# Performance work log

Measured on AMD Instinct MI355X. Metric: run time of the kernel, lower is better.

The kernel has to match this reference:

```python
import jax, jax.numpy as jnp
import numpy as np

NUM_NODES = 500000
EMB = 200        # embedding_size
U = 32           # embedding_u_size
T = 4            # edge_type_count
DIM_A = 32
B = 16384        # batch of training pairs
NN = 10          # sampled neighbors per edge type


def setup_inputs() -> dict:
    key = jax.random.key(0)
    ks = jax.random.split(key, 8)
    inv_sqrt_e = 1.0 / np.sqrt(EMB).astype(np.float32)
    return {
        "train_inputs": jax.random.randint(ks[0], (B,), 0, NUM_NODES, dtype=jnp.int32),
        "train_types": jax.random.randint(ks[1], (B,), 0, T, dtype=jnp.int32),
        "node_neigh": jax.random.randint(ks[2], (B, T, NN), 0, NUM_NODES, dtype=jnp.int32),
        # learned parameters (init matches reset_parameters)
        "node_embeddings": jax.random.uniform(ks[3], (NUM_NODES, EMB), minval=-1.0, maxval=1.0, dtype=jnp.float32),
        "node_type_embeddings": jax.random.uniform(ks[4], (NUM_NODES, T, U), minval=-1.0, maxval=1.0, dtype=jnp.float32),
        "trans_weights": jax.random.normal(ks[5], (T, U, EMB), dtype=jnp.float32) * inv_sqrt_e,
        "trans_weights_s1": jax.random.normal(ks[6], (T, U, DIM_A), dtype=jnp.float32) * inv_sqrt_e,
        "trans_weights_s2": jax.random.normal(ks[7], (T, DIM_A, 1), dtype=jnp.float32) * inv_sqrt_e,
    }


def reference(train_inputs, train_types, node_neigh,
              node_embeddings, node_type_embeddings,
              trans_weights, trans_weights_s1, trans_weights_s2):
    # Per-edge-type neighbor aggregation (copy_src + sum in the DGL code):
    # for layer l: sum_n node_type_embeddings[node_neigh[b, l, n], l, :]
    layer_idx = jnp.arange(T, dtype=node_neigh.dtype)[None, :, None]      # [1,T,1]
    neigh = node_type_embeddings[node_neigh, layer_idx, :]                # [B,T,NN,U] gather
    node_type_embed = neigh.sum(axis=2)                                   # [B,T,U]

    tw  = trans_weights[train_types]                                      # [B,U,EMB]
    tw1 = trans_weights_s1[train_types]                                   # [B,U,A]
    tw2 = trans_weights_s2[train_types][..., 0]                           # [B,A]

    # attention over edge types
    h = jnp.tanh(jnp.einsum('btu,bua->bta', node_type_embed, tw1))        # [B,T,A]
    scores = jnp.einsum('bta,ba->bt', h, tw2)                             # [B,T]
    att = jax.nn.softmax(scores, axis=1)                                  # [B,T]
    comb = jnp.einsum('bt,btu->bu', att, node_type_embed)                 # [B,U]

    node_embed = node_embeddings[train_inputs] + jnp.einsum('bu,bue->be', comb, tw)  # [B,EMB]
    norm = jnp.maximum(jnp.linalg.norm(node_embed, axis=1, keepdims=True), 1e-12)
    return node_embed / norm
```

## Files before the change

### kernel.cpp

```cpp
#include <hip/hip_runtime.h>

#define EMB 200
#define U_DIM 32
#define T_DIM 4
#define DIM_A 32
#define NN 10
#define WAVES 4

__global__ __launch_bounds__(WAVES * 64) void gatne_kernel(
    const int* __restrict__ train_inputs,
    const int* __restrict__ train_types,
    const int* __restrict__ node_neigh,
    const float* __restrict__ node_emb,
    const float* __restrict__ node_type_emb,
    const float* __restrict__ tw,
    const float* __restrict__ tw1,
    const float* __restrict__ tw2,
    float* __restrict__ out)
{
    __shared__ float s_nte[WAVES][T_DIM][U_DIM];
    __shared__ float s_comb[WAVES][U_DIM];

    const int wid  = threadIdx.x >> 6;
    const int lane = threadIdx.x & 63;
    const int u    = lane & 31;
    const int th   = lane >> 5;
    const int b    = blockIdx.x * WAVES + wid;

    const int type = train_types[b];

    int my_neigh = 0;
    if (lane < T_DIM * NN) my_neigh = node_neigh[b * T_DIM * NN + lane];

    #pragma unroll
    for (int tt = 0; tt < 2; ++tt) {
        const int t = tt * 2 + th;
        float acc = 0.f;
        #pragma unroll
        for (int n = 0; n < NN; ++n) {
            const int idx = __shfl(my_neigh, t * NN + n, 64);
            acc += node_type_emb[((long)idx * T_DIM + t) * U_DIM + u];
        }
        s_nte[wid][t][u] = acc;
    }
    __syncthreads();

    const float* tw1p = tw1 + type * U_DIM * DIM_A;
    const float  w2   = tw2[type * DIM_A + u];
    float sc[2];
    #pragma unroll
    for (int tt = 0; tt < 2; ++tt) {
        const int t = tt * 2 + th;
        float acc = 0.f;
        #pragma unroll
        for (int uu = 0; uu < U_DIM; ++uu)
            acc += s_nte[wid][t][uu] * tw1p[uu * DIM_A + u];
        float s = tanhf(acc) * w2;
        #pragma unroll
        for (int m = 1; m < 32; m <<= 1) s += __shfl_xor(s, m, 64);
        sc[tt] = s;
    }
    const float o0 = __shfl_xor(sc[0], 32, 64);
    const float o1 = __shfl_xor(sc[1], 32, 64);
    const float s0 = th ? o0    : sc[0];
    const float s1 = th ? sc[0] : o0;
    const float s2 = th ? o1    : sc[1];
    const float s3 = th ? sc[1] : o1;

    const float mx = fmaxf(fmaxf(s0, s1), fmaxf(s2, s3));
    const float e0 = expf(s0 - mx), e1 = expf(s1 - mx);
    const float e2 = expf(s2 - mx), e3 = expf(s3 - mx);
    const float inv = 1.f / (e0 + e1 + e2 + e3);

    const float comb = (e0 * s_nte[wid][0][u] + e1 * s_nte[wid][1][u] +
                        e2 * s_nte[wid][2][u] + e3 * s_nte[wid][3][u]) * inv;
    s_comb[wid][u] = comb;
    __syncthreads();

    const int    node = train_inputs[b];
    const float* twp  = tw + type * U_DIM * EMB;

    float4 v = make_float4(0.f, 0.f, 0.f, 0.f);
    float sumsq = 0.f;
    if (lane < EMB / 4) {
        v = *(const float4*)(node_emb + (long)node * EMB + lane * 4);
        #pragma unroll
        for (int uu = 0; uu < U_DIM; ++uu) {
            const float  c = s_comb[wid][uu];
            const float4 w = *(const float4*)(twp + uu * EMB + lane * 4);
            v.x += c * w.x; v.y += c * w.y; v.z += c * w.z; v.w += c * w.w;
        }
        sumsq = v.x * v.x + v.y * v.y + v.z * v.z + v.w * v.w;
    }
    #pragma unroll
    for (int m = 1; m < 64; m <<= 1) sumsq += __shfl_xor(sumsq, m, 64);

    const float rinv = 1.f / fmaxf(sqrtf(sumsq), 1e-12f);
    if (lane < EMB / 4) {
        float4 o = make_float4(v.x * rinv, v.y * rinv, v.z * rinv, v.w * rinv);
        *(float4*)(out + (long)b * EMB + lane * 4) = o;
    }
}

extern "C" void kernel_launch(void* const* d_in, const int* in_sizes, int n_in,
                              void* d_out, int out_size, void* d_ws, size_t ws_size,
                              hipStream_t stream) {
    const int*   train_inputs = (const int*)d_in[0];
    const int*   train_types  = (const int*)d_in[1];
    const int*   node_neigh   = (const int*)d_in[2];
    const float* node_emb     = (const float*)d_in[3];
    const float* node_type_e  = (const float*)d_in[4];
    const float* tw           = (const float*)d_in[5];
    const float* tw1          = (const float*)d_in[6];
    const float* tw2          = (const float*)d_in[7];
    float*       out          = (float*)d_out;

    const int B = in_sizes[0];
    const int blocks = B / WAVES;

    gatne_kernel<<<blocks, WAVES * 64, 0, stream>>>(
        train_inputs, train_types, node_neigh,
        node_emb, node_type_e, tw, tw1, tw2, out);
}
```

Baseline: 40.17 us.

## Sort batch by edge type and tile trans_weights projection over 16 rows

Splits the fused kernel into a type bucketing pass (count, prefix, scatter into a padded permutation), an attention kernel that writes the combined U-vector to workspace, and an embed kernel where each wave handles 16 same-type rows. Grouping by type lets each trans_weights load be reused across 16 rows instead of reloaded once per row. The cost is six launches instead of one, an extra round trip of the comb vectors through global memory, and 16 float4 accumulators per lane, which raises register pressure.

```diff
diff --git a/kernel.cpp b/kernel.cpp
--- a/kernel.cpp
+++ b/kernel.cpp
@@ -7,19 +7,74 @@
 #define NN 10
 #define WAVES 4
 
-__global__ __launch_bounds__(WAVES * 64) void gatne_kernel(
-    const int* __restrict__ train_inputs,
+
+__global__ __launch_bounds__(256) void k_init(int* __restrict__ perm, int* __restrict__ cnt, int pb) {
+    int i = blockIdx.x * 256 + threadIdx.x;
+    if (i < pb) perm[i] = -1;
+    if (i < 4) cnt[i] = 0;
+}
+
+__global__ __launch_bounds__(1024) void k_count(const int* __restrict__ types, int* __restrict__ cnt) {
+    __shared__ int h[4];
+    const int tid = threadIdx.x;
+    if (tid < 4) h[tid] = 0;
+    __syncthreads();
+    const int b = blockIdx.x * 1024 + tid;
+    const int ty = types[b];
+    const int lane = tid & 63;
+    #pragma unroll
+    for (int tt = 0; tt < 4; ++tt) {
+        if (ty == tt) {
+            unsigned long long m = __ballot(1);
+            if (lane == __ffsll((long long)m) - 1) atomicAdd(&h[tt], __popcll(m));
+        }
+    }
+    __syncthreads();
+    if (tid < 4) atomicAdd(&cnt[tid], h[tid]);
+}
+
+__global__ void k_base(const int* __restrict__ cnt, int* __restrict__ fill) {
+    if (threadIdx.x == 0 && blockIdx.x == 0) {
+        int f = 0;
+        #pragma unroll
+        for (int t = 0; t < 4; ++t) { fill[t] = f; f += (cnt[t] + 15) & ~15; }
+    }
+}
+
+__global__ __launch_bounds__(1024) void k_scatter(const int* __restrict__ types,
+                                                  int* __restrict__ fill, int* __restrict__ perm) {
+    __shared__ int h[4], gb[4], woff[16][4];
+    const int tid = threadIdx.x;
+    const int wv = tid >> 6, lane = tid & 63;
+    if (tid < 4) h[tid] = 0;
+    __syncthreads();
+    const int b = blockIdx.x * 1024 + tid;
+    const int ty = types[b];
+    int rank = 0;
+    #pragma unroll
+    for (int tt = 0; tt < 4; ++tt) {
+        if (ty == tt) {
+            unsigned long long m = __ballot(1);
+            rank = __popcll(m & ((1ull << lane) - 1));
+            if (lane == __ffsll((long long)m) - 1) woff[wv][tt] = atomicAdd(&h[tt], __popcll(m));
+        }
+    }
+    __syncthreads();
+    if (tid < 4) gb[tid] = atomicAdd(&fill[tid], h[tid]);
+    __syncthreads();
+    perm[gb[ty] + woff[wv][ty] + rank] = b;
+}
+
+
+__global__ __launch_bounds__(WAVES * 64) void k_comb(
     const int* __restrict__ train_types,
     const int* __restrict__ node_neigh,
-    const float* __restrict__ node_emb,
     const float* __restrict__ node_type_emb,
-    const float* __restrict__ tw,
     const float* __restrict__ tw1,
     const float* __restrict__ tw2,
-    float* __restrict__ out)
+    float* __restrict__ combw)
 {
     __shared__ float s_nte[WAVES][T_DIM][U_DIM];
-    __shared__ float s_comb[WAVES][U_DIM];
 
     const int wid  = threadIdx.x >> 6;
     const int lane = threadIdx.x & 63;
@@ -74,33 +129,90 @@
 
     const float comb = (e0 * s_nte[wid][0][u] + e1 * s_nte[wid][1][u] +
                         e2 * s_nte[wid][2][u] + e3 * s_nte[wid][3][u]) * inv;
-    s_comb[wid][u] = comb;
-    __syncthreads();
-
-    const int    node = train_inputs[b];
-    const float* twp  = tw + type * U_DIM * EMB;
-
-    float4 v = make_float4(0.f, 0.f, 0.f, 0.f);
-    float sumsq = 0.f;
-    if (lane < EMB / 4) {
-        v = *(const float4*)(node_emb + (long)node * EMB + lane * 4);
-        #pragma unroll
-        for (int uu = 0; uu < U_DIM; ++uu) {
-            const float  c = s_comb[wid][uu];
-            const float4 w = *(const float4*)(twp + uu * EMB + lane * 4);
-            v.x += c * w.x; v.y += c * w.y; v.z += c * w.z; v.w += c * w.w;
-        }
-        sumsq = v.x * v.x + v.y * v.y + v.z * v.z + v.w * v.w;
-    }
-    #pragma unroll
-    for (int m = 1; m < 64; m <<= 1) sumsq += __shfl_xor(sumsq, m, 64);
-
-    const float rinv = 1.f / fmaxf(sqrtf(sumsq), 1e-12f);
-    if (lane < EMB / 4) {
-        float4 o = make_float4(v.x * rinv, v.y * rinv, v.z * rinv, v.w * rinv);
-        *(float4*)(out + (long)b * EMB + lane * 4) = o;
-    }
-}
+    if (lane < 32) combw[(size_t)b * 32 + lane] = comb;
+}
+
+
+__global__ __launch_bounds__(WAVES * 64) void k_embed(
+    const int* __restrict__ train_inputs,
+    const int* __restrict__ train_types,
+    const int* __restrict__ perm,
+    const float* __restrict__ combw,
+    const float* __restrict__ node_emb,
+    const float* __restrict__ tw,
+    float* __restrict__ out)
+{
+    __shared__ float4 s_comb4[WAVES][16][8];
+    __shared__ int s_bg[WAVES][16];
+    __shared__ int s_node[WAVES][16];
+
+    const int wid  = threadIdx.x >> 6;
+    const int lane = threadIdx.x & 63;
+    const int g = lane >> 2, q = lane & 3;
+    const long base16 = (long)(blockIdx.x * WAVES + wid) * 16;
+
+    const int bg = perm[base16 + g];
+    const bool valid = bg >= 0;
+    float4 c0 = make_float4(0.f, 0.f, 0.f, 0.f), c1 = c0;
+    if (valid) {
+        const float4* cp = (const float4*)(combw + (size_t)bg * 32 + q * 8);
+        c0 = cp[0]; c1 = cp[1];
+    }
+    s_comb4[wid][g][q * 2]     = c0;
+    s_comb4[wid][g][q * 2 + 1] = c1;
+    if (q == 0) { s_bg[wid][g] = bg; s_node[wid][g] = valid ? train_inputs[bg] : -1; }
+    const int tyv = valid ? train_types[bg] : 0;
+    const unsigned long long vm = __ballot(valid);
+    __syncthreads();
+    if (vm == 0ull) return;
+    const int t0 = __shfl(tyv, (int)(__ffsll((long long)vm) - 1), 64);
+
+    const int  c   = lane;
+    const bool act = c < EMB / 4;
+
+    float4 nv[16];
+    #pragma unroll
+    for (int gg = 0; gg < 16; ++gg) {
+        const int nd = s_node[wid][gg];
+        float4 t = make_float4(0.f, 0.f, 0.f, 0.f);
+        if (act && nd >= 0) t = *(const float4*)(node_emb + (size_t)nd * EMB + c * 4);
+        nv[gg] = t;
+    }
+
+    const float* twp = tw + (size_t)t0 * U_DIM * EMB + c * 4;
+    const float* scp = (const float*)&s_comb4[wid][0][0];
+    float4 acc[16];
+    #pragma unroll
+    for (int gg = 0; gg < 16; ++gg) acc[gg] = make_float4(0.f, 0.f, 0.f, 0.f);
+
+    #pragma unroll 4
+    for (int uu = 0; uu < U_DIM; ++uu) {
+        float4 wv = make_float4(0.f, 0.f, 0.f, 0.f);
+        if (act) wv = *(const float4*)(twp + uu * EMB);
+        #pragma unroll
+        for (int gg = 0; gg < 16; ++gg) {
+            const float cg = scp[gg * 32 + uu];
+            acc[gg].x += cg * wv.x; acc[gg].y += cg * wv.y;
+            acc[gg].z += cg * wv.z; acc[gg].w += cg * wv.w;
+        }
+    }
+
+    #pragma unroll
+    for (int gg = 0; gg < 16; ++gg) {
+        const int bg2 = s_bg[wid][gg];
+        float4 v = make_float4(acc[gg].x + nv[gg].x, acc[gg].y + nv[gg].y,
+                               acc[gg].z + nv[gg].z, acc[gg].w + nv[gg].w);
+        float ss = v.x * v.x + v.y * v.y + v.z * v.z + v.w * v.w;
+        #pragma unroll
+        for (int m = 1; m < 64; m <<= 1) ss += __shfl_xor(ss, m, 64);
+        const float rinv = 1.f / fmaxf(sqrtf(ss), 1e-12f);
+        if (act && bg2 >= 0) {
+            float4 o = make_float4(v.x * rinv, v.y * rinv, v.z * rinv, v.w * rinv);
+            *(float4*)(out + (size_t)bg2 * EMB + c * 4) = o;
+        }
+    }
+}
+
 
 extern "C" void kernel_launch(void* const* d_in, const int* in_sizes, int n_in,
                               void* d_out, int out_size, void* d_ws, size_t ws_size,
@@ -115,10 +227,22 @@
     const float* tw2          = (const float*)d_in[7];
     float*       out          = (float*)d_out;
 
-    const int B = in_sizes[0];
-    const int blocks = B / WAVES;
-
-    gatne_kernel<<<blocks, WAVES * 64, 0, stream>>>(
-        train_inputs, train_types, node_neigh,
-        node_emb, node_type_e, tw, tw1, tw2, out);
-}
+    const int B  = in_sizes[0];
+    const int pb = B + 64;
+
+    int*   perm  = (int*)d_ws;
+    int*   cnt   = perm + pb;
+    int*   fill  = cnt + 4;
+    float* combw = (float*)d_ws + pb + 8;
+
+    k_init   <<<(pb + 255) / 256, 256, 0, stream>>>(perm, cnt, pb);
+    k_count  <<<B / 1024, 1024, 0, stream>>>(train_types, cnt);
+    k_base   <<<1, 64, 0, stream>>>(cnt, fill);
+    k_scatter<<<B / 1024, 1024, 0, stream>>>(train_types, fill, perm);
+
+    k_comb   <<<B / WAVES, WAVES * 64, 0, stream>>>(
+        train_types, node_neigh, node_type_e, tw1, tw2, combw);
+
+    k_embed  <<<pb / (16 * WAVES), WAVES * 64, 0, stream>>>(
+        train_inputs, train_types, perm, combw, node_emb, tw, out);
+}
```

Measured after the change: 53.49 us. +33.1%, slower.

## Stage trans_weights in LDS and double-buffer neighbor gathers across batch items

Applied to the files above, without the earlier changes.

Each 512-thread block now copies the whole trans_weights table (about 100 KB) into shared memory once. Each wave then processes 8 batch items in a loop, prefetching the next item's neighbor indices and node_type_emb gathers into registers while the current item's attention and projection run. This is meant to remove repeated global/L2 reads of trans_weights and hide gather latency through software pipelining. In exchange, the large LDS footprint limits each CU to one block of 8 waves, which cuts the latency hiding that occupancy provided. Every block also pays an upfront serialized table load behind a barrier. Softmax exp is switched to the fast intrinsic.

```diff
diff --git a/kernel.cpp b/kernel.cpp
--- a/kernel.cpp
+++ b/kernel.cpp
@@ -5,9 +5,12 @@
 #define T_DIM 4
 #define DIM_A 32
 #define NN 10
-#define WAVES 4
+#define BLK 512
+#define NWAVE 8
+#define BPW 8
+#define TW_FLOATS (T_DIM * U_DIM * EMB)
 
-__global__ __launch_bounds__(WAVES * 64) void gatne_kernel(
+__global__ __launch_bounds__(BLK, 2) void gatne_fused(
     const int* __restrict__ train_inputs,
     const int* __restrict__ train_types,
     const int* __restrict__ node_neigh,
@@ -18,87 +21,129 @@
     const float* __restrict__ tw2,
     float* __restrict__ out)
 {
-    __shared__ float s_nte[WAVES][T_DIM][U_DIM];
-    __shared__ float s_comb[WAVES][U_DIM];
+    __shared__ float s_tw[TW_FLOATS];
+    __shared__ float s_nte[NWAVE][T_DIM][U_DIM];
+    __shared__ float s_comb[NWAVE][U_DIM];
 
     const int wid  = threadIdx.x >> 6;
     const int lane = threadIdx.x & 63;
     const int u    = lane & 31;
     const int th   = lane >> 5;
-    const int b    = blockIdx.x * WAVES + wid;
+    const int base = blockIdx.x * (NWAVE * BPW);
 
-    const int type = train_types[b];
+    int nb[2];
+    nb[0] = (lane < T_DIM * NN) ? node_neigh[(base + wid) * T_DIM * NN + lane] : 0;
+    nb[1] = 0;
 
-    int my_neigh = 0;
-    if (lane < T_DIM * NN) my_neigh = node_neigh[b * T_DIM * NN + lane];
+    {
+        const float4* src = (const float4*)tw;
+        float4*       dst = (float4*)s_tw;
+        #pragma unroll
+        for (int k = 0; k < 13; ++k) {
+            const int i = threadIdx.x + k * BLK;
+            if (i < TW_FLOATS / 4) dst[i] = src[i];
+        }
+    }
+    __syncthreads();
+
+    float g[2][2][NN];
 
     #pragma unroll
     for (int tt = 0; tt < 2; ++tt) {
         const int t = tt * 2 + th;
-        float acc = 0.f;
         #pragma unroll
         for (int n = 0; n < NN; ++n) {
-            const int idx = __shfl(my_neigh, t * NN + n, 64);
-            acc += node_type_emb[((long)idx * T_DIM + t) * U_DIM + u];
+            const int idx = __shfl(nb[0], t * NN + n, 64);
+            g[0][tt][n] = node_type_emb[((long)idx * T_DIM + t) * U_DIM + u];
         }
-        s_nte[wid][t][u] = acc;
     }
-    __syncthreads();
 
-    const float* tw1p = tw1 + type * U_DIM * DIM_A;
-    const float  w2   = tw2[type * DIM_A + u];
-    float sc[2];
     #pragma unroll
-    for (int tt = 0; tt < 2; ++tt) {
-        const int t = tt * 2 + th;
-        float acc = 0.f;
+    for (int i = 0; i < BPW; ++i) {
+        const int cb   = i & 1;
+        const int nbuf = cb ^ 1;
+        const int b    = base + i * NWAVE + wid;
+
+        if (i + 1 < BPW)
+            nb[nbuf] = (lane < T_DIM * NN)
+                     ? node_neigh[(base + (i + 1) * NWAVE + wid) * T_DIM * NN + lane] : 0;
+
+        const int type = train_types[b];
+        const int node = train_inputs[b];
+
+        float4 nv = make_float4(0.f, 0.f, 0.f, 0.f);
+        if (lane < EMB / 4)
+            nv = *(const float4*)(node_emb + (size_t)node * EMB + lane * 4);
+
         #pragma unroll
-        for (int uu = 0; uu < U_DIM; ++uu)
-            acc += s_nte[wid][t][uu] * tw1p[uu * DIM_A + u];
-        float s = tanhf(acc) * w2;
+        for (int tt = 0; tt < 2; ++tt) {
+            const int t = tt * 2 + th;
+            float a0 = 0.f;
+            #pragma unroll
+            for (int n = 0; n < NN; ++n) a0 += g[cb][tt][n];
+            s_nte[wid][t][u] = a0;
+        }
+
+        const float* tw1p = tw1 + type * U_DIM * DIM_A;
+        const float  w2   = tw2[type * DIM_A + u];
+        float sc[2];
         #pragma unroll
-        for (int m = 1; m < 32; m <<= 1) s += __shfl_xor(s, m, 64);
-        sc[tt] = s;
-    }
-    const float o0 = __shfl_xor(sc[0], 32, 64);
-    const float o1 = __shfl_xor(sc[1], 32, 64);
-    const float s0 = th ? o0    : sc[0];
-    const float s1 = th ? sc[0] : o0;
-    const float s2 = th ? o1    : sc[1];
-    const float s3 = th ? sc[1] : o1;
+        for (int tt = 0; tt < 2; ++tt) {
+            const int t = tt * 2 + th;
+            float a1 = 0.f;
+            #pragma unroll
+            for (int uu = 0; uu < U_DIM; ++uu)
+                a1 += s_nte[wid][t][uu] * tw1p[uu * DIM_A + u];
+            float s = tanhf(a1) * w2;
+            #pragma unroll
+            for (int m = 1; m < 32; m <<= 1) s += __shfl_xor(s, m, 64);
+            sc[tt] = s;
+        }
+        const float o0 = __shfl_xor(sc[0], 32, 64);
+        const float o1 = __shfl_xor(sc[1], 32, 64);
+        const float s0 = th ? o0    : sc[0];
+        const float s1 = th ? sc[0] : o0;
+        const float s2 = th ? o1    : sc[1];
+        const float s3 = th ? sc[1] : o1;
 
-    const float mx = fmaxf(fmaxf(s0, s1), fmaxf(s2, s3));
-    const float e0 = expf(s0 - mx), e1 = expf(s1 - mx);
-    const float e2 = expf(s2 - mx), e3 = expf(s3 - mx);
-    const float inv = 1.f / (e0 + e1 + e2 + e3);
+        const float mx  = fmaxf(fmaxf(s0, s1), fmaxf(s2, s3));
+        const float e0  = __expf(s0 - mx), e1 = __expf(s1 - mx);
+        const float e2  = __expf(s2 - mx), e3 = __expf(s3 - mx);
+        const float inv = 1.f / (e0 + e1 + e2 + e3);
+        const float comb = (e0 * s_nte[wid][0][u] + e1 * s_nte[wid][1][u] +
+                            e2 * s_nte[wid][2][u] + e3 * s_nte[wid][3][u]) * inv;
+        if (lane < 32) s_comb[wid][u] = comb;
 
-    const float comb = (e0 * s_nte[wid][0][u] + e1 * s_nte[wid][1][u] +
-                        e2 * s_nte[wid][2][u] + e3 * s_nte[wid][3][u]) * inv;
-    s_comb[wid][u] = comb;
-    __syncthreads();
+        if (i + 1 < BPW) {
+            #pragma unroll
+            for (int tt = 0; tt < 2; ++tt) {
+                const int t = tt * 2 + th;
+                #pragma unroll
+                for (int n = 0; n < NN; ++n) {
+                    const int idx = __shfl(nb[nbuf], t * NN + n, 64);
+                    g[nbuf][tt][n] = node_type_emb[((long)idx * T_DIM + t) * U_DIM + u];
+                }
+            }
+        }
 
-    const int    node = train_inputs[b];
-    const float* twp  = tw + type * U_DIM * EMB;
-
-    float4 v = make_float4(0.f, 0.f, 0.f, 0.f);
-    float sumsq = 0.f;
-    if (lane < EMB / 4) {
-        v = *(const float4*)(node_emb + (long)node * EMB + lane * 4);
+        const float* twp = s_tw + type * U_DIM * EMB;
+        float4 v = nv;
+        if (lane < EMB / 4) {
+            #pragma unroll
+            for (int uu = 0; uu < U_DIM; ++uu) {
+                const float  cg = s_comb[wid][uu];
+                const float4 w  = *(const float4*)(twp + uu * EMB + lane * 4);
+                v.x += cg * w.x; v.y += cg * w.y; v.z += cg * w.z; v.w += cg * w.w;
+            }
+        }
+        float ss = (lane < EMB / 4) ? (v.x * v.x + v.y * v.y + v.z * v.z + v.w * v.w) : 0.f;
         #pragma unroll
-        for (int uu = 0; uu < U_DIM; ++uu) {
-            const float  c = s_comb[wid][uu];
-            const float4 w = *(const float4*)(twp + uu * EMB + lane * 4);
-            v.x += c * w.x; v.y += c * w.y; v.z += c * w.z; v.w += c * w.w;
+        for (int m = 1; m < 64; m <<= 1) ss += __shfl_xor(ss, m, 64);
+        const float rinv = 1.f / fmaxf(sqrtf(ss), 1e-12f);
+        if (lane < EMB / 4) {
+            float4 o = make_float4(v.x * rinv, v.y * rinv, v.z * rinv, v.w * rinv);
+            *(float4*)(out + (size_t)b * EMB + lane * 4) = o;
         }
-        sumsq = v.x * v.x + v.y * v.y + v.z * v.z + v.w * v.w;
-    }
-    #pragma unroll
-    for (int m = 1; m < 64; m <<= 1) sumsq += __shfl_xor(sumsq, m, 64);
-
-    const float rinv = 1.f / fmaxf(sqrtf(sumsq), 1e-12f);
-    if (lane < EMB / 4) {
-        float4 o = make_float4(v.x * rinv, v.y * rinv, v.z * rinv, v.w * rinv);
-        *(float4*)(out + (long)b * EMB + lane * 4) = o;
     }
 }
 
@@ -116,9 +161,9 @@
     float*       out          = (float*)d_out;
 
     const int B = in_sizes[0];
-    const int blocks = B / WAVES;
+    const int blocks = B / (NWAVE * BPW);
 
-    gatne_kernel<<<blocks, WAVES * 64, 0, stream>>>(
+    gatne_fused<<<blocks, BLK, 0, stream>>>(
         train_inputs, train_types, node_neigh,
         node_emb, node_type_e, tw, tw1, tw2, out);
 }
```

Result: faster. 36.37 us (-9.5%).

## Split into attention kernel plus type-bucketed batched embedding projection

Applied to the files above, without the earlier changes.

The single fused kernel becomes three launches. An init kernel clears the counters. A combine kernel computes the attention-combined vectors, writes them to workspace and buckets samples by edge type into striped permutation regions using atomics. An embed kernel then has each wave process 16 same-type samples, so each trans_weights row load is reused across the group through readlane broadcasts. This targets redundant per-sample weight reads, at the cost of extra launches, a workspace round trip for the combined vectors, and stripe regions that can overflow if a type/stripe bucket exceeds 2048 entries.

```diff
diff --git a/kernel.cpp b/kernel.cpp
--- a/kernel.cpp
+++ b/kernel.cpp
@@ -5,60 +5,68 @@
 #define T_DIM 4
 #define DIM_A 32
 #define NN 10
-#define WAVES 4
+#define NSTRIPE 8
+#define REGION 2048
+#define G 16
 
-__global__ __launch_bounds__(WAVES * 64) void gatne_kernel(
-    const int* __restrict__ train_inputs,
+__global__ __launch_bounds__(64) void k_init(int* __restrict__ cnt) {
+    if (threadIdx.x < T_DIM * NSTRIPE) cnt[threadIdx.x] = 0;
+}
+
+__global__ __launch_bounds__(1024, 4) void k_comb(
     const int* __restrict__ train_types,
     const int* __restrict__ node_neigh,
-    const float* __restrict__ node_emb,
     const float* __restrict__ node_type_emb,
-    const float* __restrict__ tw,
     const float* __restrict__ tw1,
     const float* __restrict__ tw2,
-    float* __restrict__ out)
+    float* __restrict__ combw,
+    int* __restrict__ cnt,
+    int* __restrict__ perm)
 {
-    __shared__ float s_nte[WAVES][T_DIM][U_DIM];
-    __shared__ float s_comb[WAVES][U_DIM];
+    __shared__ float s_nte[16][T_DIM][U_DIM];
+    __shared__ int hist[T_DIM], hbase[T_DIM];
 
-    const int wid  = threadIdx.x >> 6;
-    const int lane = threadIdx.x & 63;
-    const int u    = lane & 31;
-    const int th   = lane >> 5;
-    const int b    = blockIdx.x * WAVES + wid;
+    const int tid  = threadIdx.x;
+    const int wid  = tid >> 6, lane = tid & 63;
+    const int u    = lane & 31, th = lane >> 5;
+    const int b    = blockIdx.x * 16 + wid;
+    const int s    = blockIdx.x & (NSTRIPE - 1);
 
-    const int type = train_types[b];
+    if (tid < T_DIM) hist[tid] = 0;
+    __syncthreads();
 
-    int my_neigh = 0;
-    if (lane < T_DIM * NN) my_neigh = node_neigh[b * T_DIM * NN + lane];
+    const int ty = train_types[b];
+    int r = 0;
+    if (lane == 0) r = atomicAdd(&hist[ty], 1);
+
+    const int nb = (lane < T_DIM * NN) ? node_neigh[b * T_DIM * NN + lane] : 0;
 
     #pragma unroll
     for (int tt = 0; tt < 2; ++tt) {
         const int t = tt * 2 + th;
-        float acc = 0.f;
+        float a = 0.f;
         #pragma unroll
         for (int n = 0; n < NN; ++n) {
-            const int idx = __shfl(my_neigh, t * NN + n, 64);
-            acc += node_type_emb[((long)idx * T_DIM + t) * U_DIM + u];
+            const int idx = __shfl(nb, t * NN + n, 64);
+            a += node_type_emb[((long)idx * T_DIM + t) * U_DIM + u];
         }
-        s_nte[wid][t][u] = acc;
+        s_nte[wid][t][u] = a;
     }
-    __syncthreads();
 
-    const float* tw1p = tw1 + type * U_DIM * DIM_A;
-    const float  w2   = tw2[type * DIM_A + u];
+    const float* tw1p = tw1 + ty * U_DIM * DIM_A;
+    const float  w2   = tw2[ty * DIM_A + u];
     float sc[2];
     #pragma unroll
     for (int tt = 0; tt < 2; ++tt) {
         const int t = tt * 2 + th;
-        float acc = 0.f;
+        float a1 = 0.f;
         #pragma unroll
         for (int uu = 0; uu < U_DIM; ++uu)
-            acc += s_nte[wid][t][uu] * tw1p[uu * DIM_A + u];
-        float s = tanhf(acc) * w2;
+            a1 += s_nte[wid][t][uu] * tw1p[uu * DIM_A + u];
+        float sv = tanhf(a1) * w2;
         #pragma unroll
-        for (int m = 1; m < 32; m <<= 1) s += __shfl_xor(s, m, 64);
-        sc[tt] = s;
+        for (int m = 1; m < 32; m <<= 1) sv += __shfl_xor(sv, m, 64);
+        sc[tt] = sv;
     }
     const float o0 = __shfl_xor(sc[0], 32, 64);
     const float o1 = __shfl_xor(sc[1], 32, 64);
@@ -67,38 +75,99 @@
     const float s2 = th ? o1    : sc[1];
     const float s3 = th ? sc[1] : o1;
 
-    const float mx = fmaxf(fmaxf(s0, s1), fmaxf(s2, s3));
-    const float e0 = expf(s0 - mx), e1 = expf(s1 - mx);
-    const float e2 = expf(s2 - mx), e3 = expf(s3 - mx);
+    const float mx  = fmaxf(fmaxf(s0, s1), fmaxf(s2, s3));
+    const float e0  = __expf(s0 - mx), e1 = __expf(s1 - mx);
+    const float e2  = __expf(s2 - mx), e3 = __expf(s3 - mx);
     const float inv = 1.f / (e0 + e1 + e2 + e3);
-
     const float comb = (e0 * s_nte[wid][0][u] + e1 * s_nte[wid][1][u] +
                         e2 * s_nte[wid][2][u] + e3 * s_nte[wid][3][u]) * inv;
-    s_comb[wid][u] = comb;
+    if (lane < 32) combw[(size_t)b * 32 + u] = comb;
+
     __syncthreads();
+    if (tid < T_DIM) hbase[tid] = atomicAdd(&cnt[tid * NSTRIPE + s], hist[tid]);
+    __syncthreads();
+    if (lane == 0) perm[(ty * NSTRIPE + s) * REGION + hbase[ty] + r] = b;
+}
 
-    const int    node = train_inputs[b];
-    const float* twp  = tw + type * U_DIM * EMB;
+__global__ __launch_bounds__(256) void k_embed(
+    const int* __restrict__ train_inputs,
+    const int* __restrict__ perm,
+    const int* __restrict__ cnt,
+    const float* __restrict__ combw,
+    const float* __restrict__ node_emb,
+    const float* __restrict__ tw,
+    float* __restrict__ out)
+{
+    const int lane = threadIdx.x & 63;
+    const int wg   = blockIdx.x * 4 + (threadIdx.x >> 6);
+    const int t    = wg >> 10;
+    const int s    = (wg >> 7) & (NSTRIPE - 1);
+    const int gi   = wg & 127;
 
-    float4 v = make_float4(0.f, 0.f, 0.f, 0.f);
-    float sumsq = 0.f;
-    if (lane < EMB / 4) {
-        v = *(const float4*)(node_emb + (long)node * EMB + lane * 4);
+    const int n_all = cnt[t * NSTRIPE + s];
+    const int start = gi * G;
+    if (start >= n_all) return;
+    const int n = min(G, n_all - start);
+
+    const int base = (t * NSTRIPE + s) * REGION + start;
+
+    const int gl = lane >> 2;
+    const int q  = lane & 3;
+    int bg_l = 0;
+    if (gl < n) bg_l = perm[base + gl];
+    const int nd_l = train_inputs[bg_l];
+
+    float carr[8];
+    *(float4*)(&carr[0]) = *(const float4*)(combw + (size_t)bg_l * 32 + q * 8);
+    *(float4*)(&carr[4]) = *(const float4*)(combw + (size_t)bg_l * 32 + q * 8 + 4);
+
+    const int c  = lane;
+    const int cc = (c < 49) ? c : 49;
+
+    const float* twp = tw + (size_t)t * U_DIM * EMB + cc * 4;
+
+    float acc[G][4];
+    #pragma unroll
+    for (int g = 0; g < G; ++g) { acc[g][0] = acc[g][1] = acc[g][2] = acc[g][3] = 0.f; }
+
+    float4 wbuf[2];
+    wbuf[0] = *(const float4*)(twp);
+    #pragma unroll
+    for (int uu = 0; uu < U_DIM; ++uu) {
+        if (uu + 1 < U_DIM) wbuf[(uu + 1) & 1] = *(const float4*)(twp + (uu + 1) * EMB);
+        const float4 wv = wbuf[uu & 1];
+        const int creg = __float_as_int(carr[uu & 7]);
         #pragma unroll
-        for (int uu = 0; uu < U_DIM; ++uu) {
-            const float  c = s_comb[wid][uu];
-            const float4 w = *(const float4*)(twp + uu * EMB + lane * 4);
-            v.x += c * w.x; v.y += c * w.y; v.z += c * w.z; v.w += c * w.w;
+        for (int g = 0; g < G; ++g) {
+            const float cg = __int_as_float(
+                __builtin_amdgcn_readlane(creg, g * 4 + (uu >> 3)));
+            acc[g][0] += cg * wv.x; acc[g][1] += cg * wv.y;
+            acc[g][2] += cg * wv.z; acc[g][3] += cg * wv.w;
         }
-        sumsq = v.x * v.x + v.y * v.y + v.z * v.z + v.w * v.w;
     }
+
+    float4 nv[G];
     #pragma unroll
-    for (int m = 1; m < 64; m <<= 1) sumsq += __shfl_xor(sumsq, m, 64);
+    for (int g = 0; g < G; ++g) {
+        const int snd = __builtin_amdgcn_readlane(nd_l, g * 4);
+        nv[g] = *(const float4*)(node_emb + (size_t)snd * EMB + cc * 4);
+    }
 
-    const float rinv = 1.f / fmaxf(sqrtf(sumsq), 1e-12f);
-    if (lane < EMB / 4) {
-        float4 o = make_float4(v.x * rinv, v.y * rinv, v.z * rinv, v.w * rinv);
-        *(float4*)(out + (long)b * EMB + lane * 4) = o;
+    #pragma unroll
+    for (int g = 0; g < G; ++g) {
+        const int sbg = __builtin_amdgcn_readlane(bg_l, g * 4);
+        const float vx = acc[g][0] + nv[g].x;
+        const float vy = acc[g][1] + nv[g].y;
+        const float vz = acc[g][2] + nv[g].z;
+        const float vw = acc[g][3] + nv[g].w;
+        float ss = (c < EMB / 4) ? (vx * vx + vy * vy + vz * vz + vw * vw) : 0.f;
+        #pragma unroll
+        for (int m = 1; m < 64; m <<= 1) ss += __shfl_xor(ss, m, 64);
+        const float rinv = 1.f / fmaxf(sqrtf(ss), 1e-12f);
+        if (g < n && c < EMB / 4) {
+            float4 o = make_float4(vx * rinv, vy * rinv, vz * rinv, vw * rinv);
+            *(float4*)(out + (size_t)sbg * EMB + c * 4) = o;
+        }
     }
 }
 
@@ -116,9 +185,14 @@
     float*       out          = (float*)d_out;
 
     const int B = in_sizes[0];
-    const int blocks = B / WAVES;
 
-    gatne_kernel<<<blocks, WAVES * 64, 0, stream>>>(
-        train_inputs, train_types, node_neigh,
-        node_emb, node_type_e, tw, tw1, tw2, out);
+    int*   cnt   = (int*)d_ws;
+    int*   perm  = cnt + T_DIM * NSTRIPE;
+    float* combw = (float*)(perm + T_DIM * NSTRIPE * REGION);
+
+    k_init<<<1, 64, 0, stream>>>(cnt);
+    k_comb<<<B / 16, 1024, 0, stream>>>(
+        train_types, node_neigh, node_type_e, tw1, tw2, combw, cnt, perm);
+    k_embed<<<(T_DIM * NSTRIPE * (REGION / G)) / 4, 256, 0, stream>>>(
+        train_inputs, perm, cnt, combw, node_emb, tw, out);
 }
```

After: 78.86 us. +96.3%, slower.
